# Optimization experiments

Hardware: AMD Instinct MI355X
Metric: run time of the kernel (lower is better)

## Reference

```python
import jax, jax.numpy as jnp
import numpy as np
from jax import lax

NGTH = 15  # num_gth_mem
EPS = 1e-5  # BatchNorm eps


def _conv(x, w, b):
    y = lax.conv_general_dilated(x, w, (1, 1), 'VALID',
                                 dimension_numbers=('NCHW', 'OIHW', 'NCHW'))
    return y + b[None, :, None, None]


def _bn(x, g, b, m, v):
    # eval-mode BatchNorm2d with running stats
    return g[None, :, None, None] * (x - m[None, :, None, None]) * lax.rsqrt(v[None, :, None, None] + EPS) + b[None, :, None, None]


def _masked_stats(x, w):
    # x: (B, M, ...) ; w: (B, M) float weights. Population mean/std over masked mem slots.
    extra = (1,) * (x.ndim - 2)
    we = w.reshape(w.shape[:2] + extra)
    cnt = jnp.sum(w, axis=1).reshape((w.shape[0],) + extra)
    s = jnp.sum(x * we, axis=1)
    ss = jnp.sum(x * x * we, axis=1)
    mean = s / cnt
    var = jnp.maximum(ss / cnt - mean * mean, 0.0)
    return mean, jnp.sqrt(var)


def _forward(target_scores, ptm, pmt, predicted_iou, mem_mask, params):
    nf, ns, nmem, c, h, w = ptm.shape
    B = nf * ns
    ts = target_scores.reshape(B, 1, h, w)
    pmt = pmt.reshape(B, nmem, 1, h, w)
    ptm = ptm.reshape(B, nmem, c, h, w)
    mask = mem_mask.reshape(B, nmem)
    piou = predicted_iou.reshape(B, 1, 1, 1)

    mf = mask.astype(ts.dtype)
    # rank of each selected slot within the masked (ordered) selection
    rank = jnp.cumsum(mf, axis=1) - 1.0
    gth_w = mf * (rank < NGTH).astype(ts.dtype)   # first NGTH selected slots
    oth_w = mf * (rank >= NGTH).astype(ts.dtype)  # remaining selected slots

    max_ts = jnp.max(ts.reshape(B, -1), axis=1)

    pmt_mean, pmt_std = _masked_stats(pmt, mf)                 # (B,1,h,w)
    pmt_gth = pmt[:, :NGTH]                                    # unmasked slice (as in torch code)
    pmt_gth_mean = jnp.mean(pmt_gth, axis=1)
    pmt_gth_std = jnp.std(pmt_gth, axis=1)
    pmt_oth_mean, pmt_oth_std = _masked_stats(pmt, oth_w)

    ptm_max = jnp.max(ptm.reshape(B, nmem, -1), axis=2)        # (B, nmem)
    m_mm, s_mm = _masked_stats(ptm_max, mf)
    m_gm, s_gm = _masked_stats(ptm_max, gth_w)
    m_om, s_om = _masked_stats(ptm_max, oth_w)

    def bcast(v):
        return jnp.broadcast_to(v.reshape(B, 1, 1, 1), (B, 1, h, w))

    inp = jnp.concatenate([
        bcast(max_ts), jnp.broadcast_to(piou, (B, 1, h, w)),
        pmt_mean, pmt_std, pmt_gth_mean, pmt_gth_std, pmt_oth_mean, pmt_oth_std,
        bcast(m_mm), bcast(s_mm), bcast(m_gm), bcast(s_gm), bcast(m_om), bcast(s_om)
    ], axis=1)  # (B, 14, h, w)

    (c1w, c1b, g1, b1, m1, v1, c2w, c2b, g2, b2, m2, v2,
     c3w, c3b, g3, b3, m3, v3, c4w, c4b) = params
    x = jax.nn.relu(_bn(_conv(inp, c1w, c1b), g1, b1, m1, v1))
    x = lax.reduce_window(x, -jnp.inf, lax.max, (1, 1, 2, 2), (1, 1, 2, 2), 'VALID')
    x = jax.nn.relu(_bn(_conv(x, c2w, c2b), g2, b2, m2, v2))
    x = jax.nn.relu(_bn(_conv(x, c3w, c3b), g3, b3, m3, v3))
    x = _conv(x, c4w, c4b)
    return jnp.max(x, axis=(2, 3), keepdims=True)  # AdaptiveMaxPool2d((1,1)) -> (B,1,1,1)


def setup_inputs() -> dict:
    key = jax.random.key(0)
    ks = jax.random.split(key, 16)
    nf, ns, nmem, h, w = 16, 32, 30, 32, 32
    d = {}
    d['target_scores'] = jax.random.normal(ks[0], (nf, ns, 1, h, w), jnp.float32)
    d['ptm'] = jax.random.uniform(ks[1], (nf, ns, nmem, 1, h, w), jnp.float32)
    d['pmt'] = jax.random.uniform(ks[2], (nf, ns, nmem, 1, h, w), jnp.float32)
    d['predicted_iou'] = jax.random.uniform(ks[3], (nf, ns), jnp.float32)
    mask = jax.random.uniform(ks[4], (nf, ns, nmem)) < 0.7
    mask = mask.at[..., :20].set(True)  # >= 20 selected -> 'other' set non-empty
    d['mem_mask'] = mask
    d['conv1_w'] = jax.random.normal(ks[5], (64, 14, 3, 3), jnp.float32) * 0.1
    d['conv1_b'] = jnp.zeros((64,), jnp.float32)
    d['bn1_g'] = jnp.ones((64,), jnp.float32); d['bn1_b'] = jnp.zeros((64,), jnp.float32)
    d['bn1_m'] = jnp.zeros((64,), jnp.float32); d['bn1_v'] = jnp.ones((64,), jnp.float32)
    d['conv2_w'] = jax.random.normal(ks[6], (64, 64, 3, 3), jnp.float32) * 0.05
    d['conv2_b'] = jnp.zeros((64,), jnp.float32)
    d['bn2_g'] = jnp.ones((64,), jnp.float32); d['bn2_b'] = jnp.zeros((64,), jnp.float32)
    d['bn2_m'] = jnp.zeros((64,), jnp.float32); d['bn2_v'] = jnp.ones((64,), jnp.float32)
    d['conv3_w'] = jax.random.normal(ks[7], (64, 64, 3, 3), jnp.float32) * 0.05
    d['conv3_b'] = jnp.zeros((64,), jnp.float32)
    d['bn3_g'] = jnp.ones((64,), jnp.float32); d['bn3_b'] = jnp.zeros((64,), jnp.float32)
    d['bn3_m'] = jnp.zeros((64,), jnp.float32); d['bn3_v'] = jnp.ones((64,), jnp.float32)
    d['conv4_w'] = jax.random.normal(ks[8], (1, 64, 3, 3), jnp.float32) * 0.05
    d['conv4_b'] = jnp.zeros((1,), jnp.float32)
    return d


def reference(target_scores, ptm, pmt, predicted_iou, mem_mask,
              conv1_w, conv1_b, bn1_g, bn1_b, bn1_m, bn1_v,
              conv2_w, conv2_b, bn2_g, bn2_b, bn2_m, bn2_v,
              conv3_w, conv3_b, bn3_g, bn3_b, bn3_m, bn3_v,
              conv4_w, conv4_b):
    params = (conv1_w, conv1_b, bn1_g, bn1_b, bn1_m, bn1_v,
              conv2_w, conv2_b, bn2_g, bn2_b, bn2_m, bn2_v,
              conv3_w, conv3_b, bn3_g, bn3_b, bn3_m, bn3_v,
              conv4_w, conv4_b)
    return _forward(target_scores, ptm, pmt, predicted_iou, mem_mask, params)
```

## Files before the change

kernel.cpp:

```cpp
#include <hip/hip_runtime.h>
#include <math.h>

#define NFB  512
#define NMEM 30
#define PIX  1024
#define EPSF 1e-5f

typedef _Float16 half8_t __attribute__((ext_vector_type(8)));
typedef _Float16 half4_t __attribute__((ext_vector_type(4)));
typedef float float4_t __attribute__((ext_vector_type(4)));

#define OFF_W2R   13631488
#define OFF_W3R   13705216
#define OFF_WR1   13778944
#define OFF_WSUM1 13791232

__global__ __launch_bounds__(256) void k_prep(
    const float* __restrict__ c1w, const float* __restrict__ c2w,
    const float* __restrict__ c3w, _Float16* __restrict__ w2rep,
    _Float16* __restrict__ w3rep, _Float16* __restrict__ wr1,
    float* __restrict__ wsum1)
{
  int i = blockIdx.x * 256 + threadIdx.x;
  if (i < 36864) {
    int kr = i / 12288, rem = i - kr * 12288;
    int oc = rem / 192, k = rem - oc * 192;
    int kc = k >> 6, ci = k & 63;
    w2rep[i] = (_Float16)c2w[((oc * 64 + ci) * 3 + kr) * 3 + kc];
  } else if (i < 73728) {
    int j = i - 36864;
    int kr = j / 12288, rem = j - kr * 12288;
    int oc = rem / 192, k = rem - oc * 192;
    int kc = k >> 6, ci = k & 63;
    w3rep[j] = (_Float16)c3w[((oc * 64 + ci) * 3 + kr) * 3 + kc];
  } else if (i < 79872) {
    int j = i - 73728;
    int kr = j / 2048, rem = j - kr * 2048;
    int oc = rem >> 5, k = rem & 31;
    int kc = k >> 3, ci = k & 7;
    _Float16 v = (_Float16)0.f;
    if (kc < 3 && ci < 6)
      v = (_Float16)c1w[((oc * 14 + (2 + ci)) * 3 + kr) * 3 + kc];
    wr1[j] = v;
  } else if (i < 80384) {
    int j = i - 79872;
    int oc = j >> 3, u = j & 7;
    const int uch[8] = {0, 1, 8, 9, 10, 11, 12, 13};
    const float* wp = c1w + (oc * 14 + uch[u]) * 9;
    float s = 0.f;
    #pragma unroll
    for (int k = 0; k < 9; ++k) s += wp[k];
    wsum1[j] = s;
  }
}

#define PROC_CHUNK(CC, BASE, N)                                     \
  _Pragma("unroll")                                                 \
  for (int j = 0; j < (N); ++j) {                                   \
    const int mj = (BASE) + j;                                      \
    float wm = ((mwm >> mj) & 1u) ? 1.f : 0.f;                      \
    float wo = ((mwo >> mj) & 1u) ? 1.f : 0.f;                      \
    float xv[4] = {CC[j].x, CC[j].y, CC[j].z, CC[j].w};             \
    _Pragma("unroll")                                               \
    for (int k = 0; k < 4; ++k) {                                   \
      float x = xv[k];                                              \
      sA[k] = fmaf(wm, x, sA[k]); qA[k] = fmaf(wm * x, x, qA[k]);   \
      sO[k] = fmaf(wo, x, sO[k]); qO[k] = fmaf(wo * x, x, qO[k]);   \
      if (mj < 15) { sG[k] += x; qG[k] = fmaf(x, x, qG[k]); }       \
    }                                                               \
  }

__global__ __launch_bounds__(256, 2) void k_mega(
    const float* __restrict__ ts, const float* __restrict__ ptm,
    const float* __restrict__ pmt, const float* __restrict__ piou,
    const int* __restrict__ mask,
    const _Float16* __restrict__ wr1, const float* __restrict__ wsum1,
    const float* __restrict__ c1b, const float* __restrict__ g1,
    const float* __restrict__ b1, const float* __restrict__ m1,
    const float* __restrict__ v1,
    const _Float16* __restrict__ w2rep,
    const float* __restrict__ c2b, const float* __restrict__ g2,
    const float* __restrict__ b2, const float* __restrict__ m2,
    const float* __restrict__ v2,
    const _Float16* __restrict__ w3rep,
    const float* __restrict__ c3b, const float* __restrict__ g3,
    const float* __restrict__ b3, const float* __restrict__ m3,
    const float* __restrict__ v3,
    const float* __restrict__ c4w, const float* __restrict__ c4b,
    float* __restrict__ out)
{
  __shared__ __align__(16) char s_buf[55296];
  __shared__ float s_wm[NMEM], s_wo[NMEM], s_pmax[NMEM];
  __shared__ float s_red[4], s_scal[12], s_cnt[4];
  __shared__ unsigned s_mbits[2];
  __shared__ float s_w4[576];

  const int b = blockIdx.x, t = threadIdx.x;
  const int lane = t & 63, wave = t >> 6;
  const int n16 = lane & 15, q = lane >> 4;
  _Float16* const IMG = (_Float16*)s_buf;
  _Float16* const X1  = (_Float16*)(s_buf + 16448);
  _Float16* const X2S = (_Float16*)s_buf;
  _Float16* const X3  = (_Float16*)(s_buf + 29952);

  for (int i = t; i < 576; i += 256) {
    int ci = i / 9, k = i - ci * 9;
    s_w4[k * 64 + ci] = c4w[i];
  }
  if (t == 0) {
    float cum = 0.f, cm = 0.f, cg = 0.f, co = 0.f;
    unsigned bm = 0u, bo = 0u;
    for (int m = 0; m < NMEM; ++m) {
      float f  = (mask[b * NMEM + m] != 0) ? 1.f : 0.f;
      float gg = (cum < 15.f) ? f : 0.f;
      float oo = f - gg;
      cum += f;
      s_wm[m] = f; s_wo[m] = oo;
      if (f > 0.5f)  bm |= (1u << m);
      if (oo > 0.5f) bo |= (1u << m);
      cm += f; cg += gg; co += oo;
    }
    s_cnt[0] = cm; s_cnt[1] = cg; s_cnt[2] = co;
    s_mbits[0] = bm; s_mbits[1] = bo;
  }
  {
    const float* pb = ptm + (size_t)b * NMEM * PIX + lane * 4;
    #pragma unroll
    for (int pass = 0; pass < 2; ++pass) {
      float4 u[4][4];
      #pragma unroll
      for (int k = 0; k < 4; ++k) {
        int m = wave + 4 * (pass * 4 + k);
        if (m < NMEM) {
          #pragma unroll
          for (int j = 0; j < 4; ++j)
            u[k][j] = *(const float4*)(pb + (size_t)m * PIX + j * 256);
        }
      }
      #pragma unroll
      for (int k = 0; k < 4; ++k) {
        int m = wave + 4 * (pass * 4 + k);
        if (m < NMEM) {
          float4 v0 = u[k][0], v1_ = u[k][1], v2_ = u[k][2], v3_ = u[k][3];
          float mx = fmaxf(fmaxf(fmaxf(v0.x, v0.y), fmaxf(v0.z, v0.w)),
                           fmaxf(fmaxf(v1_.x, v1_.y), fmaxf(v1_.z, v1_.w)));
          mx = fmaxf(mx, fmaxf(fmaxf(fmaxf(v2_.x, v2_.y), fmaxf(v2_.z, v2_.w)),
                               fmaxf(fmaxf(v3_.x, v3_.y), fmaxf(v3_.z, v3_.w))));
          #pragma unroll
          for (int off = 32; off > 0; off >>= 1)
            mx = fmaxf(mx, __shfl_down(mx, off, 64));
          if (lane == 0) s_pmax[m] = mx;
        }
      }
    }
  }
  {
    float4 v = ((const float4*)(ts + (size_t)b * PIX))[t];
    float mx = fmaxf(fmaxf(v.x, v.y), fmaxf(v.z, v.w));
    #pragma unroll
    for (int off = 32; off > 0; off >>= 1)
      mx = fmaxf(mx, __shfl_down(mx, off, 64));
    if (lane == 0) s_red[wave] = mx;
  }
  __syncthreads();
  if (t == 0) {
    float maxts = fmaxf(fmaxf(s_red[0], s_red[1]), fmaxf(s_red[2], s_red[3]));
    float sm = 0, sm2 = 0, sg = 0, sg2 = 0, so = 0, so2 = 0;
    for (int m = 0; m < NMEM; ++m) {
      float x = s_pmax[m];
      float gg = s_wm[m] - s_wo[m];
      sm += s_wm[m] * x;  sm2 += s_wm[m] * x * x;
      sg += gg * x;       sg2 += gg * x * x;
      so += s_wo[m] * x;  so2 += s_wo[m] * x * x;
    }
    float cm = s_cnt[0], cg = s_cnt[1], co = s_cnt[2];
    float a = sm / cm, g = sg / cg, o = so / co;
    s_scal[0] = maxts; s_scal[1] = piou[b];
    s_scal[2] = a; s_scal[3] = sqrtf(fmaxf(sm2 / cm - a * a, 0.f));
    s_scal[4] = g; s_scal[5] = sqrtf(fmaxf(sg2 / cg - g * g, 0.f));
    s_scal[6] = o; s_scal[7] = sqrtf(fmaxf(so2 / co - o * o, 0.f));
  }
  {
    const unsigned mwm = s_mbits[0], mwo = s_mbits[1];
    const float cm = s_cnt[0], co = s_cnt[2];
    const int p0 = t * 4;
    const float* pb = pmt + (size_t)b * NMEM * PIX + p0;
    float sA[4] = {0,0,0,0}, qA[4] = {0,0,0,0};
    float sG[4] = {0,0,0,0}, qG[4] = {0,0,0,0};
    float sO[4] = {0,0,0,0}, qO[4] = {0,0,0,0};
    float4 c0[6], c1[6], c2[6], c3[6], c4[6];
    #pragma unroll
    for (int j = 0; j < 6; ++j) c0[j] = *(const float4*)(pb + (size_t)j * PIX);
    #pragma unroll
    for (int j = 0; j < 6; ++j) c1[j] = *(const float4*)(pb + (size_t)(6 + j) * PIX);
    PROC_CHUNK(c0, 0, 6)
    #pragma unroll
    for (int j = 0; j < 6; ++j) c2[j] = *(const float4*)(pb + (size_t)(12 + j) * PIX);
    PROC_CHUNK(c1, 6, 6)
    #pragma unroll
    for (int j = 0; j < 6; ++j) c3[j] = *(const float4*)(pb + (size_t)(18 + j) * PIX);
    PROC_CHUNK(c2, 12, 6)
    #pragma unroll
    for (int j = 0; j < 6; ++j) c4[j] = *(const float4*)(pb + (size_t)(24 + j) * PIX);
    PROC_CHUNK(c3, 18, 6)
    PROC_CHUNK(c4, 24, 6)
    half8_t* ob = (half8_t*)(IMG) + p0;
    #pragma unroll
    for (int j = 0; j < 4; ++j) {
      float m0 = sA[j] / cm;   float d0 = sqrtf(fmaxf(qA[j] / cm - m0 * m0, 0.f));
      float m1_ = sG[j] / 15.f; float d1 = sqrtf(fmaxf(qG[j] / 15.f - m1_ * m1_, 0.f));
      float m2_ = sO[j] / co;   float d2 = sqrtf(fmaxf(qO[j] / co - m2_ * m2_, 0.f));
      half8_t v;
      v[0] = (_Float16)m0;  v[1] = (_Float16)d0;
      v[2] = (_Float16)m1_; v[3] = (_Float16)d1;
      v[4] = (_Float16)m2_; v[5] = (_Float16)d2;
      v[6] = (_Float16)0.f; v[7] = (_Float16)0.f;
      ob[j] = v;
    }
    if (t < 4) {
      half8_t z = {(_Float16)0.f,(_Float16)0.f,(_Float16)0.f,(_Float16)0.f,
                   (_Float16)0.f,(_Float16)0.f,(_Float16)0.f,(_Float16)0.f};
      ((half8_t*)IMG)[1024 + t] = z;
    }
  }
  __syncthreads();

  {
    const int ocA = wave * 16 + n16;
    half8_t af[3];
    #pragma unroll
    for (int kr = 0; kr < 3; ++kr)
      af[kr] = *(const half8_t*)(wr1 + (kr * 64 + ocA) * 32 + q * 8);
    const int oc0 = wave * 16 + q * 4;
    float scv[4], shv[4], cst[4];
    #pragma unroll
    for (int rg = 0; rg < 4; ++rg) {
      int oc = oc0 + rg;
      float s = g1[oc] * rsqrtf(v1[oc] + EPSF);
      scv[rg] = s;
      shv[rg] = (c1b[oc] - m1[oc]) * s + b1[oc];
      float c = 0.f;
      #pragma unroll
      for (int u = 0; u < 8; ++u) c = fmaf(wsum1[oc * 8 + u], s_scal[u], c);
      cst[rg] = c;
    }
    #pragma unroll 1
    for (int pr = 0; pr < 15; ++pr) {
      const int r0 = pr * 2;
      float4_t acc[2][2];
      #pragma unroll
      for (int row = 0; row < 2; ++row)
        #pragma unroll
        for (int tt = 0; tt < 2; ++tt)
          acc[row][tt] = (float4_t){0.f, 0.f, 0.f, 0.f};
      #pragma unroll
      for (int row = 0; row < 2; ++row) {
        #pragma unroll
        for (int kr = 0; kr < 3; ++kr) {
          const int ip = (r0 + row + kr) * 32 + n16 + q;
          #pragma unroll
          for (int tt = 0; tt < 2; ++tt) {
            half8_t bf = *(const half8_t*)(IMG + (ip + tt * 16) * 8);
            acc[row][tt] = __builtin_amdgcn_mfma_f32_16x16x32_f16(
                af[kr], bf, acc[row][tt], 0, 0, 0);
          }
        }
      }
      #pragma unroll
      for (int tt = 0; tt < 2; ++tt) {
        float mm[4];
        #pragma unroll
        for (int j = 0; j < 4; ++j) {
          float m = fmaxf(acc[0][tt][j], acc[1][tt][j]);
          mm[j] = fmaxf(m, __shfl_xor(m, 1, 64));
        }
        if ((n16 & 1) == 0) {
          int pc = tt * 8 + (n16 >> 1);
          half4_t vv;
          if (pc < 15) {
            #pragma unroll
            for (int rg = 0; rg < 4; ++rg)
              vv[rg] = (_Float16)fmaxf(scv[rg] * (mm[rg] + cst[rg]) + shv[rg], 0.f);
          } else {
            vv[0] = (_Float16)0.f; vv[1] = (_Float16)0.f;
            vv[2] = (_Float16)0.f; vv[3] = (_Float16)0.f;
          }
          *(half4_t*)(X1 + (pr * 16 + pc) * 72 + oc0) = vv;
        }
      }
    }
  }
  __syncthreads();

  {
    int base72[11];
    #pragma unroll
    for (int nt = 0; nt < 11; ++nt) {
      int p = nt * 16 + n16;
      int pe = (p < 169) ? p : 168;
      int r = pe / 13, c = pe - r * 13;
      base72[nt] = (r * 16 + c) * 72;
    }
    float4_t acc[11];
    #pragma unroll
    for (int nt = 0; nt < 11; ++nt) acc[nt] = (float4_t){0.f, 0.f, 0.f, 0.f};
    const int ocA = wave * 16 + n16;

    auto mfma_kr = [&](const half8_t (&af)[6], int kr) {
      const int krbase = kr * (16 * 72);
      #pragma unroll
      for (int ks = 0; ks < 6; ++ks) {
        const int k0 = ks * 32 + q * 8;
        const int kadd = krbase + (k0 >> 6) * 72 + (k0 & 63);
        #pragma unroll
        for (int nt = 0; nt < 11; ++nt) {
          half8_t bf = *(const half8_t*)(X1 + base72[nt] + kadd);
          acc[nt] = __builtin_amdgcn_mfma_f32_16x16x32_f16(af[ks], bf, acc[nt], 0, 0, 0);
        }
      }
    };

    half8_t afA[6], afB[6];
    {
      const half8_t* wp = (const half8_t*)(w2rep + (size_t)(0 * 64 + ocA) * 192 + q * 8);
      #pragma unroll
      for (int ks = 0; ks < 6; ++ks) afA[ks] = wp[ks * 4];
    }
    {
      const half8_t* wp = (const half8_t*)(w2rep + (size_t)(1 * 64 + ocA) * 192 + q * 8);
      #pragma unroll
      for (int ks = 0; ks < 6; ++ks) afB[ks] = wp[ks * 4];
      mfma_kr(afA, 0);
    }
    {
      const half8_t* wp = (const half8_t*)(w2rep + (size_t)(2 * 64 + ocA) * 192 + q * 8);
      #pragma unroll
      for (int ks = 0; ks < 6; ++ks) afA[ks] = wp[ks * 4];
      mfma_kr(afB, 1);
    }
    mfma_kr(afA, 2);

    const int ocb = wave * 16 + q * 4;
    float scv[4], shv[4];
    #pragma unroll
    for (int rg = 0; rg < 4; ++rg) {
      int o = ocb + rg;
      float s = g2[o] * rsqrtf(v2[o] + EPSF);
      scv[rg] = s;
      shv[rg] = (c2b[o] - m2[o]) * s + b2[o];
    }
    half4_t vout[11];
    #pragma unroll
    for (int nt = 0; nt < 11; ++nt) {
      #pragma unroll
      for (int rg = 0; rg < 4; ++rg)
        vout[nt][rg] = (_Float16)fmaxf(acc[nt][rg] * scv[rg] + shv[rg], 0.f);
    }
    __syncthreads();
    #pragma unroll
    for (int nt = 0; nt < 11; ++nt) {
      int p = nt * 16 + n16;
      if (p < 169) {
        int r = p / 13, c = p - r * 13;
        *(half4_t*)(X2S + (r * 16 + c) * 72 + ocb) = vout[nt];
      }
    }
  }
  __syncthreads();

  {
    int base72[8];
    #pragma unroll
    for (int nt = 0; nt < 8; ++nt) {
      int p = nt * 16 + n16;
      int pe = (p < 121) ? p : 120;
      int r = pe / 11, c = pe - r * 11;
      base72[nt] = (r * 16 + c) * 72;
    }
    float4_t acc[8];
    #pragma unroll
    for (int nt = 0; nt < 8; ++nt) acc[nt] = (float4_t){0.f, 0.f, 0.f, 0.f};
    const int ocA = wave * 16 + n16;

    auto mfma_kr3 = [&](const half8_t (&af)[6], int kr) {
      const int krbase = kr * (16 * 72);
      #pragma unroll
      for (int ks = 0; ks < 6; ++ks) {
        const int k0 = ks * 32 + q * 8;
        const int kadd = krbase + (k0 >> 6) * 72 + (k0 & 63);
        #pragma unroll
        for (int nt = 0; nt < 8; ++nt) {
          half8_t bf = *(const half8_t*)(X2S + base72[nt] + kadd);
          acc[nt] = __builtin_amdgcn_mfma_f32_16x16x32_f16(af[ks], bf, acc[nt], 0, 0, 0);
        }
      }
    };

    half8_t afA[6], afB[6];
    {
      const half8_t* wp = (const half8_t*)(w3rep + (size_t)(0 * 64 + ocA) * 192 + q * 8);
      #pragma unroll
      for (int ks = 0; ks < 6; ++ks) afA[ks] = wp[ks * 4];
    }
    {
      const half8_t* wp = (const half8_t*)(w3rep + (size_t)(1 * 64 + ocA) * 192 + q * 8);
      #pragma unroll
      for (int ks = 0; ks < 6; ++ks) afB[ks] = wp[ks * 4];
      mfma_kr3(afA, 0);
    }
    {
      const half8_t* wp = (const half8_t*)(w3rep + (size_t)(2 * 64 + ocA) * 192 + q * 8);
      #pragma unroll
      for (int ks = 0; ks < 6; ++ks) afA[ks] = wp[ks * 4];
      mfma_kr3(afB, 1);
    }
    mfma_kr3(afA, 2);

    const int ocb = wave * 16 + q * 4;
    float scv[4], shv[4];
    #pragma unroll
    for (int rg = 0; rg < 4; ++rg) {
      int o = ocb + rg;
      float s = g3[o] * rsqrtf(v3[o] + EPSF);
      scv[rg] = s;
      shv[rg] = (c3b[o] - m3[o]) * s + b3[o];
    }
    #pragma unroll
    for (int nt = 0; nt < 8; ++nt) {
      int p = nt * 16 + n16;
      if (p < 121) {
        int r = p / 11, c = p - r * 11;
        half4_t vv;
        #pragma unroll
        for (int rg = 0; rg < 4; ++rg)
          vv[rg] = (_Float16)fmaxf(acc[nt][rg] * scv[rg] + shv[rg], 0.f);
        *(half4_t*)(X3 + (r * 16 + c) * 72 + ocb) = vv;
      }
    }
  }
  __syncthreads();

  {
    float val = -INFINITY;
    if (t < 81) {
      const int r = t / 9, c = t - (t / 9) * 9;
      float acc = 0.f;
      #pragma unroll
      for (int kr = 0; kr < 3; ++kr)
        #pragma unroll
        for (int kc = 0; kc < 3; ++kc) {
          const _Float16* ip = X3 + ((r + kr) * 16 + (c + kc)) * 72;
          const float* wk = s_w4 + (kr * 3 + kc) * 64;
          #pragma unroll
          for (int cig = 0; cig < 8; ++cig) {
            half8_t x = *(const half8_t*)(ip + cig * 8);
            #pragma unroll
            for (int j = 0; j < 8; ++j)
              acc = fmaf((float)x[j], wk[cig * 8 + j], acc);
          }
        }
      val = acc;
    }
    #pragma unroll
    for (int off = 32; off > 0; off >>= 1)
      val = fmaxf(val, __shfl_down(val, off, 64));
    if (lane == 0) s_red[wave] = val;
    __syncthreads();
    if (t == 0)
      out[b] = fmaxf(fmaxf(s_red[0], s_red[1]), fmaxf(s_red[2], s_red[3])) + c4b[0];
  }
}

extern "C" void kernel_launch(void* const* d_in, const int* in_sizes, int n_in,
                              void* d_out, int out_size, void* d_ws, size_t ws_size,
                              hipStream_t stream) {
  const float* ts   = (const float*)d_in[0];
  const float* ptm  = (const float*)d_in[1];
  const float* pmt  = (const float*)d_in[2];
  const float* piou = (const float*)d_in[3];
  const int*   mask = (const int*)d_in[4];
  const float* c1w = (const float*)d_in[5];
  const float* c1b = (const float*)d_in[6];
  const float* g1  = (const float*)d_in[7];
  const float* b1  = (const float*)d_in[8];
  const float* m1  = (const float*)d_in[9];
  const float* v1  = (const float*)d_in[10];
  const float* c2w = (const float*)d_in[11];
  const float* c2b = (const float*)d_in[12];
  const float* g2  = (const float*)d_in[13];
  const float* b2  = (const float*)d_in[14];
  const float* m2  = (const float*)d_in[15];
  const float* v2  = (const float*)d_in[16];
  const float* c3w = (const float*)d_in[17];
  const float* c3b = (const float*)d_in[18];
  const float* g3  = (const float*)d_in[19];
  const float* b3  = (const float*)d_in[20];
  const float* m3  = (const float*)d_in[21];
  const float* v3  = (const float*)d_in[22];
  const float* c4w = (const float*)d_in[23];
  const float* c4b = (const float*)d_in[24];

  char* ws = (char*)d_ws;
  _Float16*  w2rep = (_Float16*)(ws + OFF_W2R);
  _Float16*  w3rep = (_Float16*)(ws + OFF_W3R);
  _Float16*  wr1   = (_Float16*)(ws + OFF_WR1);
  float*     wsum1 = (float*)(ws + OFF_WSUM1);

  k_prep<<<314, 256, 0, stream>>>(c1w, c2w, c3w, w2rep, w3rep, wr1, wsum1);
  k_mega<<<NFB, 256, 0, stream>>>(
      ts, ptm, pmt, piou, mask,
      wr1, wsum1, c1b, g1, b1, m1, v1,
      w2rep, c2b, g2, b2, m2, v2,
      w3rep, c3b, g3, b3, m3, v3,
      c4w, c4b, (float*)d_out);
}
```

Baseline: 228.4 us.

## Split stats phase into separate wide kernel and stage image via global workspace

```diff
diff --git a/kernel.cpp b/kernel.cpp
--- a/kernel.cpp
+++ b/kernel.cpp
@@ -10,70 +10,191 @@
 typedef _Float16 half4_t __attribute__((ext_vector_type(4)));
 typedef float float4_t __attribute__((ext_vector_type(4)));
 
+#define OFF_SCAL  8388608
 #define OFF_W2R   13631488
 #define OFF_W3R   13705216
 #define OFF_WR1   13778944
 #define OFF_WSUM1 13791232
 
-__global__ __launch_bounds__(256) void k_prep(
-    const float* __restrict__ c1w, const float* __restrict__ c2w,
-    const float* __restrict__ c3w, _Float16* __restrict__ w2rep,
-    _Float16* __restrict__ w3rep, _Float16* __restrict__ wr1,
-    float* __restrict__ wsum1)
-{
-  int i = blockIdx.x * 256 + threadIdx.x;
-  if (i < 36864) {
-    int kr = i / 12288, rem = i - kr * 12288;
-    int oc = rem / 192, k = rem - oc * 192;
-    int kc = k >> 6, ci = k & 63;
-    w2rep[i] = (_Float16)c2w[((oc * 64 + ci) * 3 + kr) * 3 + kc];
-  } else if (i < 73728) {
-    int j = i - 36864;
-    int kr = j / 12288, rem = j - kr * 12288;
-    int oc = rem / 192, k = rem - oc * 192;
-    int kc = k >> 6, ci = k & 63;
-    w3rep[j] = (_Float16)c3w[((oc * 64 + ci) * 3 + kr) * 3 + kc];
-  } else if (i < 79872) {
-    int j = i - 73728;
-    int kr = j / 2048, rem = j - kr * 2048;
-    int oc = rem >> 5, k = rem & 31;
-    int kc = k >> 3, ci = k & 7;
-    _Float16 v = (_Float16)0.f;
-    if (kc < 3 && ci < 6)
-      v = (_Float16)c1w[((oc * 14 + (2 + ci)) * 3 + kr) * 3 + kc];
-    wr1[j] = v;
-  } else if (i < 80384) {
-    int j = i - 79872;
-    int oc = j >> 3, u = j & 7;
-    const int uch[8] = {0, 1, 8, 9, 10, 11, 12, 13};
-    const float* wp = c1w + (oc * 14 + uch[u]) * 9;
-    float s = 0.f;
-    #pragma unroll
-    for (int k = 0; k < 9; ++k) s += wp[k];
-    wsum1[j] = s;
-  }
-}
-
-#define PROC_CHUNK(CC, BASE, N)                                     \
-  _Pragma("unroll")                                                 \
-  for (int j = 0; j < (N); ++j) {                                   \
-    const int mj = (BASE) + j;                                      \
-    float wm = ((mwm >> mj) & 1u) ? 1.f : 0.f;                      \
-    float wo = ((mwo >> mj) & 1u) ? 1.f : 0.f;                      \
-    float xv[4] = {CC[j].x, CC[j].y, CC[j].z, CC[j].w};             \
-    _Pragma("unroll")                                               \
-    for (int k = 0; k < 4; ++k) {                                   \
-      float x = xv[k];                                              \
-      sA[k] = fmaf(wm, x, sA[k]); qA[k] = fmaf(wm * x, x, qA[k]);   \
-      sO[k] = fmaf(wo, x, sO[k]); qO[k] = fmaf(wo * x, x, qO[k]);   \
-      if (mj < 15) { sG[k] += x; qG[k] = fmaf(x, x, qG[k]); }       \
-    }                                                               \
-  }
-
-__global__ __launch_bounds__(256, 2) void k_mega(
+#define PROC2(CC, BASE)                                              \
+  _Pragma("unroll")                                                  \
+  for (int j = 0; j < 10; ++j) {                                     \
+    const int mj = (BASE) + j;                                       \
+    float wm = ((mwm >> mj) & 1u) ? 1.f : 0.f;                       \
+    float wo = ((mwo >> mj) & 1u) ? 1.f : 0.f;                       \
+    float xv[2] = {CC[j].x, CC[j].y};                                \
+    _Pragma("unroll")                                                \
+    for (int k = 0; k < 2; ++k) {                                    \
+      float x = xv[k];                                               \
+      sA[k] = fmaf(wm, x, sA[k]); qA[k] = fmaf(wm * x, x, qA[k]);    \
+      sO[k] = fmaf(wo, x, sO[k]); qO[k] = fmaf(wo * x, x, qO[k]);    \
+      if (mj < 15) { sG[k] += x; qG[k] = fmaf(x, x, qG[k]); }        \
+    }                                                                \
+  }
+
+__global__ __launch_bounds__(256) void k_stats(
     const float* __restrict__ ts, const float* __restrict__ ptm,
     const float* __restrict__ pmt, const float* __restrict__ piou,
     const int* __restrict__ mask,
+    const float* __restrict__ c1w, const float* __restrict__ c2w,
+    const float* __restrict__ c3w,
+    _Float16* __restrict__ w2rep, _Float16* __restrict__ w3rep,
+    _Float16* __restrict__ wr1, float* __restrict__ wsum1,
+    _Float16* __restrict__ img, float* __restrict__ scal)
+{
+  __shared__ float s_pmax[NMEM];
+  __shared__ float s_red[4];
+  const int bid = blockIdx.x, t = threadIdx.x;
+
+  if (bid < 314) {
+    int i = bid * 256 + t;
+    if (i < 36864) {
+      int kr = i / 12288, rem = i - kr * 12288;
+      int oc = rem / 192, k = rem - oc * 192;
+      int kc = k >> 6, ci = k & 63;
+      w2rep[i] = (_Float16)c2w[((oc * 64 + ci) * 3 + kr) * 3 + kc];
+    } else if (i < 73728) {
+      int j = i - 36864;
+      int kr = j / 12288, rem = j - kr * 12288;
+      int oc = rem / 192, k = rem - oc * 192;
+      int kc = k >> 6, ci = k & 63;
+      w3rep[j] = (_Float16)c3w[((oc * 64 + ci) * 3 + kr) * 3 + kc];
+    } else if (i < 79872) {
+      int j = i - 73728;
+      int kr = j / 2048, rem = j - kr * 2048;
+      int oc = rem >> 5, k = rem & 31;
+      int kc = k >> 3, ci = k & 7;
+      _Float16 v = (_Float16)0.f;
+      if (kc < 3 && ci < 6)
+        v = (_Float16)c1w[((oc * 14 + (2 + ci)) * 3 + kr) * 3 + kc];
+      wr1[j] = v;
+    } else if (i < 80384) {
+      int j = i - 79872;
+      int oc = j >> 3, u = j & 7;
+      const int uch[8] = {0, 1, 8, 9, 10, 11, 12, 13};
+      const float* wp = c1w + (oc * 14 + uch[u]) * 9;
+      float s = 0.f;
+      #pragma unroll
+      for (int k = 0; k < 9; ++k) s += wp[k];
+      wsum1[j] = s;
+    }
+    return;
+  }
+
+  if (bid < 826) {
+    const int b = bid - 314;
+    const int lane = t & 63, wave = t >> 6;
+    {
+      const float* pb = ptm + (size_t)b * NMEM * PIX + lane * 4;
+      #pragma unroll
+      for (int pass = 0; pass < 2; ++pass) {
+        float4 u[4][4];
+        #pragma unroll
+        for (int k = 0; k < 4; ++k) {
+          int m = wave + 4 * (pass * 4 + k);
+          if (m < NMEM) {
+            #pragma unroll
+            for (int j = 0; j < 4; ++j)
+              u[k][j] = *(const float4*)(pb + (size_t)m * PIX + j * 256);
+          }
+        }
+        #pragma unroll
+        for (int k = 0; k < 4; ++k) {
+          int m = wave + 4 * (pass * 4 + k);
+          if (m < NMEM) {
+            float4 v0 = u[k][0], v1_ = u[k][1], v2_ = u[k][2], v3_ = u[k][3];
+            float mx = fmaxf(fmaxf(fmaxf(v0.x, v0.y), fmaxf(v0.z, v0.w)),
+                             fmaxf(fmaxf(v1_.x, v1_.y), fmaxf(v1_.z, v1_.w)));
+            mx = fmaxf(mx, fmaxf(fmaxf(fmaxf(v2_.x, v2_.y), fmaxf(v2_.z, v2_.w)),
+                                 fmaxf(fmaxf(v3_.x, v3_.y), fmaxf(v3_.z, v3_.w))));
+            #pragma unroll
+            for (int off = 32; off > 0; off >>= 1)
+              mx = fmaxf(mx, __shfl_down(mx, off, 64));
+            if (lane == 0) s_pmax[m] = mx;
+          }
+        }
+      }
+    }
+    {
+      float4 v = ((const float4*)(ts + (size_t)b * PIX))[t];
+      float mx = fmaxf(fmaxf(v.x, v.y), fmaxf(v.z, v.w));
+      #pragma unroll
+      for (int off = 32; off > 0; off >>= 1)
+        mx = fmaxf(mx, __shfl_down(mx, off, 64));
+      if (lane == 0) s_red[wave] = mx;
+    }
+    __syncthreads();
+    if (t == 0) {
+      float maxts = fmaxf(fmaxf(s_red[0], s_red[1]), fmaxf(s_red[2], s_red[3]));
+      float cum = 0.f, cm = 0.f, cg = 0.f, co = 0.f;
+      float sm = 0, sm2 = 0, sg = 0, sg2 = 0, so = 0, so2 = 0;
+      for (int m = 0; m < NMEM; ++m) {
+        float f  = (mask[b * NMEM + m] != 0) ? 1.f : 0.f;
+        float gg = (cum < 15.f) ? f : 0.f;
+        float oo = f - gg;
+        cum += f;
+        float x = s_pmax[m];
+        sm += f * x;  sm2 += f * x * x;
+        sg += gg * x; sg2 += gg * x * x;
+        so += oo * x; so2 += oo * x * x;
+        cm += f; cg += gg; co += oo;
+      }
+      float a = sm / cm, g = sg / cg, o = so / co;
+      float* sc = scal + b * 8;
+      sc[0] = maxts; sc[1] = piou[b];
+      sc[2] = a; sc[3] = sqrtf(fmaxf(sm2 / cm - a * a, 0.f));
+      sc[4] = g; sc[5] = sqrtf(fmaxf(sg2 / cg - g * g, 0.f));
+      sc[6] = o; sc[7] = sqrtf(fmaxf(so2 / co - o * o, 0.f));
+    }
+    return;
+  }
+
+  {
+    const int j0 = bid - 826;
+    const int b = j0 >> 1;
+    const int px0 = (j0 & 1) * 512 + t * 2;
+    const float* pb = pmt + (size_t)b * NMEM * PIX + px0;
+    float2 ca[10], cb[10];
+    #pragma unroll
+    for (int j = 0; j < 10; ++j) ca[j] = *(const float2*)(pb + (size_t)j * PIX);
+    #pragma unroll
+    for (int j = 0; j < 10; ++j) cb[j] = *(const float2*)(pb + (size_t)(10 + j) * PIX);
+    unsigned mwm = 0u, mwo = 0u;
+    float cum = 0.f, cm = 0.f, co = 0.f;
+    for (int m = 0; m < NMEM; ++m) {
+      int f = (mask[b * NMEM + m] != 0) ? 1 : 0;
+      int oo = (f && (cum >= 15.f)) ? 1 : 0;
+      cum += (float)f;
+      if (f)  mwm |= (1u << m);
+      if (oo) mwo |= (1u << m);
+      cm += (float)f; co += (float)oo;
+    }
+    float sA[2] = {0,0}, qA[2] = {0,0};
+    float sG[2] = {0,0}, qG[2] = {0,0};
+    float sO[2] = {0,0}, qO[2] = {0,0};
+    PROC2(ca, 0)
+    #pragma unroll
+    for (int j = 0; j < 10; ++j) ca[j] = *(const float2*)(pb + (size_t)(20 + j) * PIX);
+    PROC2(cb, 10)
+    PROC2(ca, 20)
+    half8_t* ob = (half8_t*)img + (size_t)b * 1024 + px0;
+    #pragma unroll
+    for (int k = 0; k < 2; ++k) {
+      float m0 = sA[k] / cm;    float d0 = sqrtf(fmaxf(qA[k] / cm - m0 * m0, 0.f));
+      float m1_ = sG[k] / 15.f; float d1 = sqrtf(fmaxf(qG[k] / 15.f - m1_ * m1_, 0.f));
+      float m2_ = sO[k] / co;   float d2 = sqrtf(fmaxf(qO[k] / co - m2_ * m2_, 0.f));
+      half8_t v;
+      v[0] = (_Float16)m0;  v[1] = (_Float16)d0;
+      v[2] = (_Float16)m1_; v[3] = (_Float16)d1;
+      v[4] = (_Float16)m2_; v[5] = (_Float16)d2;
+      v[6] = (_Float16)0.f; v[7] = (_Float16)0.f;
+      ob[k] = v;
+    }
+  }
+}
+
+__global__ __launch_bounds__(256, 2) void k_conv(
+    const _Float16* __restrict__ img, const float* __restrict__ scal,
     const _Float16* __restrict__ wr1, const float* __restrict__ wsum1,
     const float* __restrict__ c1b, const float* __restrict__ g1,
     const float* __restrict__ b1, const float* __restrict__ m1,
@@ -89,139 +210,27 @@
     const float* __restrict__ c4w, const float* __restrict__ c4b,
     float* __restrict__ out)
 {
-  __shared__ __align__(16) char s_buf[55296];
-  __shared__ float s_wm[NMEM], s_wo[NMEM], s_pmax[NMEM];
-  __shared__ float s_red[4], s_scal[12], s_cnt[4];
-  __shared__ unsigned s_mbits[2];
-  __shared__ float s_w4[576];
+  __shared__ __align__(16) char s_buf[54144];
+  __shared__ float s_red[4], s_scal[8];
 
   const int b = blockIdx.x, t = threadIdx.x;
   const int lane = t & 63, wave = t >> 6;
   const int n16 = lane & 15, q = lane >> 4;
   _Float16* const IMG = (_Float16*)s_buf;
-  _Float16* const X1  = (_Float16*)(s_buf + 16448);
+  _Float16* const X1  = (_Float16*)(s_buf + 16432);
   _Float16* const X2S = (_Float16*)s_buf;
-  _Float16* const X3  = (_Float16*)(s_buf + 29952);
-
-  for (int i = t; i < 576; i += 256) {
-    int ci = i / 9, k = i - ci * 9;
-    s_w4[k * 64 + ci] = c4w[i];
-  }
-  if (t == 0) {
-    float cum = 0.f, cm = 0.f, cg = 0.f, co = 0.f;
-    unsigned bm = 0u, bo = 0u;
-    for (int m = 0; m < NMEM; ++m) {
-      float f  = (mask[b * NMEM + m] != 0) ? 1.f : 0.f;
-      float gg = (cum < 15.f) ? f : 0.f;
-      float oo = f - gg;
-      cum += f;
-      s_wm[m] = f; s_wo[m] = oo;
-      if (f > 0.5f)  bm |= (1u << m);
-      if (oo > 0.5f) bo |= (1u << m);
-      cm += f; cg += gg; co += oo;
-    }
-    s_cnt[0] = cm; s_cnt[1] = cg; s_cnt[2] = co;
-    s_mbits[0] = bm; s_mbits[1] = bo;
-  }
-  {
-    const float* pb = ptm + (size_t)b * NMEM * PIX + lane * 4;
-    #pragma unroll
-    for (int pass = 0; pass < 2; ++pass) {
-      float4 u[4][4];
-      #pragma unroll
-      for (int k = 0; k < 4; ++k) {
-        int m = wave + 4 * (pass * 4 + k);
-        if (m < NMEM) {
-          #pragma unroll
-          for (int j = 0; j < 4; ++j)
-            u[k][j] = *(const float4*)(pb + (size_t)m * PIX + j * 256);
-        }
-      }
-      #pragma unroll
-      for (int k = 0; k < 4; ++k) {
-        int m = wave + 4 * (pass * 4 + k);
-        if (m < NMEM) {
-          float4 v0 = u[k][0], v1_ = u[k][1], v2_ = u[k][2], v3_ = u[k][3];
-          float mx = fmaxf(fmaxf(fmaxf(v0.x, v0.y), fmaxf(v0.z, v0.w)),
-                           fmaxf(fmaxf(v1_.x, v1_.y), fmaxf(v1_.z, v1_.w)));
-          mx = fmaxf(mx, fmaxf(fmaxf(fmaxf(v2_.x, v2_.y), fmaxf(v2_.z, v2_.w)),
-                               fmaxf(fmaxf(v3_.x, v3_.y), fmaxf(v3_.z, v3_.w))));
-          #pragma unroll
-          for (int off = 32; off > 0; off >>= 1)
-            mx = fmaxf(mx, __shfl_down(mx, off, 64));
-          if (lane == 0) s_pmax[m] = mx;
-        }
-      }
-    }
-  }
-  {
-    float4 v = ((const float4*)(ts + (size_t)b * PIX))[t];
-    float mx = fmaxf(fmaxf(v.x, v.y), fmaxf(v.z, v.w));
-    #pragma unroll
-    for (int off = 32; off > 0; off >>= 1)
-      mx = fmaxf(mx, __shfl_down(mx, off, 64));
-    if (lane == 0) s_red[wave] = mx;
-  }
-  __syncthreads();
-  if (t == 0) {
-    float maxts = fmaxf(fmaxf(s_red[0], s_red[1]), fmaxf(s_red[2], s_red[3]));
-    float sm = 0, sm2 = 0, sg = 0, sg2 = 0, so = 0, so2 = 0;
-    for (int m = 0; m < NMEM; ++m) {
-      float x = s_pmax[m];
-      float gg = s_wm[m] - s_wo[m];
-      sm += s_wm[m] * x;  sm2 += s_wm[m] * x * x;
-      sg += gg * x;       sg2 += gg * x * x;
-      so += s_wo[m] * x;  so2 += s_wo[m] * x * x;
-    }
-    float cm = s_cnt[0], cg = s_cnt[1], co = s_cnt[2];
-    float a = sm / cm, g = sg / cg, o = so / co;
-    s_scal[0] = maxts; s_scal[1] = piou[b];
-    s_scal[2] = a; s_scal[3] = sqrtf(fmaxf(sm2 / cm - a * a, 0.f));
-    s_scal[4] = g; s_scal[5] = sqrtf(fmaxf(sg2 / cg - g * g, 0.f));
-    s_scal[6] = o; s_scal[7] = sqrtf(fmaxf(so2 / co - o * o, 0.f));
-  }
-  {
-    const unsigned mwm = s_mbits[0], mwo = s_mbits[1];
-    const float cm = s_cnt[0], co = s_cnt[2];
-    const int p0 = t * 4;
-    const float* pb = pmt + (size_t)b * NMEM * PIX + p0;
-    float sA[4] = {0,0,0,0}, qA[4] = {0,0,0,0};
-    float sG[4] = {0,0,0,0}, qG[4] = {0,0,0,0};
-    float sO[4] = {0,0,0,0}, qO[4] = {0,0,0,0};
-    float4 c0[6], c1[6], c2[6], c3[6], c4[6];
-    #pragma unroll
-    for (int j = 0; j < 6; ++j) c0[j] = *(const float4*)(pb + (size_t)j * PIX);
-    #pragma unroll
-    for (int j = 0; j < 6; ++j) c1[j] = *(const float4*)(pb + (size_t)(6 + j) * PIX);
-    PROC_CHUNK(c0, 0, 6)
-    #pragma unroll
-    for (int j = 0; j < 6; ++j) c2[j] = *(const float4*)(pb + (size_t)(12 + j) * PIX);
-    PROC_CHUNK(c1, 6, 6)
-    #pragma unroll
-    for (int j = 0; j < 6; ++j) c3[j] = *(const float4*)(pb + (size_t)(18 + j) * PIX);
-    PROC_CHUNK(c2, 12, 6)
-    #pragma unroll
-    for (int j = 0; j < 6; ++j) c4[j] = *(const float4*)(pb + (size_t)(24 + j) * PIX);
-    PROC_CHUNK(c3, 18, 6)
-    PROC_CHUNK(c4, 24, 6)
-    half8_t* ob = (half8_t*)(IMG) + p0;
-    #pragma unroll
-    for (int j = 0; j < 4; ++j) {
-      float m0 = sA[j] / cm;   float d0 = sqrtf(fmaxf(qA[j] / cm - m0 * m0, 0.f));
-      float m1_ = sG[j] / 15.f; float d1 = sqrtf(fmaxf(qG[j] / 15.f - m1_ * m1_, 0.f));
-      float m2_ = sO[j] / co;   float d2 = sqrtf(fmaxf(qO[j] / co - m2_ * m2_, 0.f));
-      half8_t v;
-      v[0] = (_Float16)m0;  v[1] = (_Float16)d0;
-      v[2] = (_Float16)m1_; v[3] = (_Float16)d1;
-      v[4] = (_Float16)m2_; v[5] = (_Float16)d2;
-      v[6] = (_Float16)0.f; v[7] = (_Float16)0.f;
-      ob[j] = v;
-    }
-    if (t < 4) {
-      half8_t z = {(_Float16)0.f,(_Float16)0.f,(_Float16)0.f,(_Float16)0.f,
+  _Float16* const X3  = (_Float16*)(s_buf + 29520);
+
+  {
+    const half8_t* src = (const half8_t*)img + (size_t)b * 1024;
+    half8_t* dst = (half8_t*)IMG;
+    for (int i = t; i < 1027; i += 256) {
+      half8_t v = {(_Float16)0.f,(_Float16)0.f,(_Float16)0.f,(_Float16)0.f,
                    (_Float16)0.f,(_Float16)0.f,(_Float16)0.f,(_Float16)0.f};
-      ((half8_t*)IMG)[1024 + t] = z;
-    }
+      if (i < 1024) v = src[i];
+      dst[i] = v;
+    }
+    if (t < 8) s_scal[t] = scal[b * 8 + t];
   }
   __syncthreads();
 
@@ -274,17 +283,12 @@
           float m = fmaxf(acc[0][tt][j], acc[1][tt][j]);
           mm[j] = fmaxf(m, __shfl_xor(m, 1, 64));
         }
-        if ((n16 & 1) == 0) {
-          int pc = tt * 8 + (n16 >> 1);
+        int pc = tt * 8 + (n16 >> 1);
+        if (((n16 & 1) == 0) && pc < 15) {
           half4_t vv;
-          if (pc < 15) {
-            #pragma unroll
-            for (int rg = 0; rg < 4; ++rg)
-              vv[rg] = (_Float16)fmaxf(scv[rg] * (mm[rg] + cst[rg]) + shv[rg], 0.f);
-          } else {
-            vv[0] = (_Float16)0.f; vv[1] = (_Float16)0.f;
-            vv[2] = (_Float16)0.f; vv[3] = (_Float16)0.f;
-          }
+          #pragma unroll
+          for (int rg = 0; rg < 4; ++rg)
+            vv[rg] = (_Float16)fmaxf(scv[rg] * (mm[rg] + cst[rg]) + shv[rg], 0.f);
           *(half4_t*)(X1 + (pr * 16 + pc) * 72 + oc0) = vv;
         }
       }
@@ -368,6 +372,10 @@
   }
   __syncthreads();
 
+  float w4r0 = c4w[t];
+  float w4r1 = c4w[256 + t];
+  float w4r2 = (t < 64) ? c4w[512 + t] : 0.f;
+
   {
     int base72[8];
     #pragma unroll
@@ -441,6 +449,15 @@
   __syncthreads();
 
   {
+    float* w4s = (float*)s_buf;
+    int i0 = t;        { int ci = i0 / 9, k = i0 - ci * 9; w4s[k * 64 + ci] = w4r0; }
+    int i1 = 256 + t;  { int ci = i1 / 9, k = i1 - ci * 9; w4s[k * 64 + ci] = w4r1; }
+    if (t < 64) { int i2 = 512 + t; int ci = i2 / 9, k = i2 - ci * 9; w4s[k * 64 + ci] = w4r2; }
+  }
+  __syncthreads();
+
+  {
+    const float* w4s = (const float*)s_buf;
     float val = -INFINITY;
     if (t < 81) {
       const int r = t / 9, c = t - (t / 9) * 9;
@@ -450,7 +467,7 @@
         #pragma unroll
         for (int kc = 0; kc < 3; ++kc) {
           const _Float16* ip = X3 + ((r + kr) * 16 + (c + kc)) * 72;
-          const float* wk = s_w4 + (kr * 3 + kc) * 64;
+          const float* wk = w4s + (kr * 3 + kc) * 64;
           #pragma unroll
           for (int cig = 0; cig < 8; ++cig) {
             half8_t x = *(const half8_t*)(ip + cig * 8);
@@ -501,15 +518,18 @@
   const float* c4b = (const float*)d_in[24];
 
   char* ws = (char*)d_ws;
+  _Float16*  img   = (_Float16*)ws;
+  float*     scal  = (float*)(ws + OFF_SCAL);
   _Float16*  w2rep = (_Float16*)(ws + OFF_W2R);
   _Float16*  w3rep = (_Float16*)(ws + OFF_W3R);
   _Float16*  wr1   = (_Float16*)(ws + OFF_WR1);
   float*     wsum1 = (float*)(ws + OFF_WSUM1);
 
-  k_prep<<<314, 256, 0, stream>>>(c1w, c2w, c3w, w2rep, w3rep, wr1, wsum1);
-  k_mega<<<NFB, 256, 0, stream>>>(
-      ts, ptm, pmt, piou, mask,
-      wr1, wsum1, c1b, g1, b1, m1, v1,
+  k_stats<<<1850, 256, 0, stream>>>(
+      ts, ptm, pmt, piou, mask, c1w, c2w, c3w,
+      w2rep, w3rep, wr1, wsum1, img, scal);
+  k_conv<<<NFB, 256, 0, stream>>>(
+      img, scal, wr1, wsum1, c1b, g1, b1, m1, v1,
       w2rep, c2b, g2, b2, m2, v2,
       w3rep, c3b, g3, b3, m3, v3,
       c4w, c4b, (float*)d_out);
```

New measurement: 221.3 us. -3.1%, faster.
